# Kernel tuning notes

Hardware: AMD Instinct MI355X
Metric: run time of the kernel (lower is better)

The kernel has to match this reference:

```python
import jax, jax.numpy as jnp
import numpy as np

N_GROUP = 8
TOPK_GROUP = 4
TOP_K = 8
ROUTED_SCALING = 2.5
NUM_EXPERTS = 256
HIDDEN = 7168
TOKENS = 8192


def setup_inputs() -> dict:
    key = jax.random.key(0)
    k1, k2, k3 = jax.random.split(key, 3)
    hidden_states = jax.random.normal(k1, (TOKENS, HIDDEN), dtype=jnp.float32)
    weight = jax.random.normal(k2, (NUM_EXPERTS, HIDDEN), dtype=jnp.float32) * 0.02
    e_score_correction_bias = jax.random.normal(k3, (NUM_EXPERTS,), dtype=jnp.float32) * 0.1
    return {"hidden_states": hidden_states, "weight": weight,
            "e_score_correction_bias": e_score_correction_bias}


def reference(hidden_states, weight, e_score_correction_bias):
    # logits = x @ W^T  (fp32 gate GEMM)
    logits = jnp.einsum('th,eh->te', hidden_states.astype(jnp.float32), weight)
    scores = jax.nn.sigmoid(logits)                       # [T, E]
    swb = scores + e_score_correction_bias                # [T, E]
    T, E = swb.shape
    gsize = E // N_GROUP
    # per-group score = sum of top-2 biased scores within each group
    grouped = swb.reshape(T, N_GROUP, gsize)
    top2, _ = jax.lax.top_k(grouped, 2)                   # [T, G, 2]
    group_scores = top2.sum(axis=-1)                      # [T, G]
    # keep topk_group groups
    _, gidx = jax.lax.top_k(group_scores, TOPK_GROUP)     # [T, topk_group]
    rows = jnp.arange(T)[:, None]
    group_mask = jnp.zeros((T, N_GROUP), jnp.float32).at[rows, gidx].set(1.0)
    score_mask = jnp.repeat(group_mask, gsize, axis=-1)   # [T, E]
    swb_masked = swb * score_mask
    # top_k experts among kept groups
    _, tidx = jax.lax.top_k(swb_masked, TOP_K)            # [T, top_k]
    new_mask = jnp.zeros((T, E), jnp.float32).at[rows, tidx].set(1.0)
    sel = scores * new_mask
    score_sum = sel.sum(axis=-1, keepdims=True) + 1e-20
    return sel / score_sum * ROUTED_SCALING
```

## Files before the change

### kernel.cpp

```cpp
#include <hip/hip_runtime.h>
#include <math.h>

#define TOKENS   8192
#define HIDDEN   7168
#define NEXPERT  256
#define NGROUP   8
#define TOPKG    4
#define TOPK     8
#define SCALE    2.5f

#define BM 128
#define BN 128
#define BK 32
#define KSPLIT 4
#define KPB (HIDDEN / KSPLIT)
#define NT  (KPB / BK)

#define RSTR 72

typedef _Float16 half8 __attribute__((ext_vector_type(8)));
typedef _Float16 half4 __attribute__((ext_vector_type(4)));
typedef float    floatx4 __attribute__((ext_vector_type(4)));

__device__ __forceinline__ void cvt_store(_Float16* __restrict__ H,
                                          int row, int k0, float4 v) {
    half4 h, l;
    h[0] = (_Float16)v.x; h[1] = (_Float16)v.y;
    h[2] = (_Float16)v.z; h[3] = (_Float16)v.w;
    l[0] = (_Float16)(v.x - (float)h[0]);
    l[1] = (_Float16)(v.y - (float)h[1]);
    l[2] = (_Float16)(v.z - (float)h[2]);
    l[3] = (_Float16)(v.w - (float)h[3]);
    const int base = row * RSTR + ((k0 >> 3) << 4) + (k0 & 7);
    *(half4*)&H[base]     = h;
    *(half4*)&H[base + 8] = l;
}

__global__ __launch_bounds__(256) void zero_kernel(float* __restrict__ O) {
    const int i = blockIdx.x * 256 + threadIdx.x;
    *(float4*)&O[(size_t)i * 4] = float4{0.f, 0.f, 0.f, 0.f};
}

__global__ __launch_bounds__(256, 2) void gate_gemm_kernel(
    const float* __restrict__ X, const float* __restrict__ W,
    float* __restrict__ OUT)
{
    __shared__ _Float16 Ab[2][BM * RSTR];
    __shared__ _Float16 Bb[2][BN * RSTR];

    const int tid = threadIdx.x;
    const int nb  = blockIdx.x * BN;
    const int mb  = blockIdx.y * BM;
    const int kb  = blockIdx.z * KPB;

    const int srow = tid >> 3;
    const int sk0  = (tid & 7) * 4;
    const float* Aptr = X + (size_t)(mb + srow) * HIDDEN + kb + sk0;
    const float* Bptr = W + (size_t)(nb + srow) * HIDDEN + kb + sk0;

    float4 av[4], bv[4];
#pragma unroll
    for (int q = 0; q < 4; q++) {
        av[q] = *(const float4*)(Aptr + (size_t)(q * 32) * HIDDEN);
        bv[q] = *(const float4*)(Bptr + (size_t)(q * 32) * HIDDEN);
    }
#pragma unroll
    for (int q = 0; q < 4; q++) {
        cvt_store(Ab[0], q * 32 + srow, sk0, av[q]);
        cvt_store(Bb[0], q * 32 + srow, sk0, bv[q]);
    }

    const int lane = tid & 63, wave = tid >> 6;
    const int wm = (wave >> 1) * 64, wn = (wave & 1) * 64;
    const int fr = lane & 15, quad = lane >> 4;

    floatx4 acc[4][4];
#pragma unroll
    for (int i = 0; i < 4; i++)
#pragma unroll
        for (int j = 0; j < 4; j++) acc[i][j] = floatx4{0.f, 0.f, 0.f, 0.f};

    for (int t = 0; t < NT; t++) {
        if (t + 1 < NT) {
            const int o = (t + 1) * BK;
#pragma unroll
            for (int q = 0; q < 4; q++) {
                av[q] = *(const float4*)(Aptr + o + (size_t)(q * 32) * HIDDEN);
                bv[q] = *(const float4*)(Bptr + o + (size_t)(q * 32) * HIDDEN);
            }
        }

        __syncthreads();

        const _Float16* __restrict__ Ac = Ab[t & 1];
        const _Float16* __restrict__ Bc = Bb[t & 1];

        half8 ah[4], al[4];
#pragma unroll
        for (int i = 0; i < 4; i++) {
            const int a = (wm + i * 16 + fr) * RSTR + quad * 16;
            ah[i] = *(const half8*)&Ac[a];
            al[i] = *(const half8*)&Ac[a + 8];
        }
#pragma unroll
        for (int j = 0; j < 4; j++) {
            const int b = (wn + j * 16 + fr) * RSTR + quad * 16;
            const half8 bh = *(const half8*)&Bc[b];
            const half8 bl = *(const half8*)&Bc[b + 8];
#pragma unroll
            for (int i = 0; i < 4; i++) {
                acc[i][j] = __builtin_amdgcn_mfma_f32_16x16x32_f16(
                    al[i], bh, acc[i][j], 0, 0, 0);
                acc[i][j] = __builtin_amdgcn_mfma_f32_16x16x32_f16(
                    ah[i], bl, acc[i][j], 0, 0, 0);
                acc[i][j] = __builtin_amdgcn_mfma_f32_16x16x32_f16(
                    ah[i], bh, acc[i][j], 0, 0, 0);
            }
        }

        if (t + 1 < NT) {
            _Float16* An = Ab[(t + 1) & 1];
            _Float16* Bn = Bb[(t + 1) & 1];
#pragma unroll
            for (int q = 0; q < 4; q++) {
                cvt_store(An, q * 32 + srow, sk0, av[q]);
                cvt_store(Bn, q * 32 + srow, sk0, bv[q]);
            }
        }
    }

#pragma unroll
    for (int i = 0; i < 4; i++)
#pragma unroll
        for (int j = 0; j < 4; j++) {
            const int col = nb + wn + j * 16 + fr;
#pragma unroll
            for (int r = 0; r < 4; r++) {
                const int row = mb + wm + i * 16 + quad * 4 + r;
                atomicAdd(&OUT[(size_t)row * NEXPERT + col], acc[i][j][r]);
            }
        }
}

__global__ __launch_bounds__(256) void route_kernel(
    float* __restrict__ S, const float* __restrict__ bias)
{
    const int lane = threadIdx.x & 63;
    const int wave = threadIdx.x >> 6;
    const int t    = blockIdx.x * 4 + wave;

    const float4 lg4 = *(const float4*)&S[(size_t)t * NEXPERT + lane * 4];
    const float4 b4  = *(const float4*)&bias[lane * 4];
    float sc[4];
    sc[0] = 1.0f / (1.0f + expf(-lg4.x));
    sc[1] = 1.0f / (1.0f + expf(-lg4.y));
    sc[2] = 1.0f / (1.0f + expf(-lg4.z));
    sc[3] = 1.0f / (1.0f + expf(-lg4.w));
    float swb[4] = { sc[0] + b4.x, sc[1] + b4.y, sc[2] + b4.z, sc[3] + b4.w };

    float m1 = -INFINITY, m2 = -INFINITY;
#pragma unroll
    for (int j = 0; j < 4; j++) {
        const float v = swb[j];
        if (v > m1)      { m2 = m1; m1 = v; }
        else if (v > m2) { m2 = v; }
    }
#pragma unroll
    for (int s = 1; s < 8; s <<= 1) {
        const float o1 = __shfl_xor(m1, s, 64);
        const float o2 = __shfl_xor(m2, s, 64);
        const float hi = fmaxf(m1, o1);
        const float lo = fminf(m1, o1);
        m2 = fmaxf(lo, fmaxf(m2, o2));
        m1 = hi;
    }
    const float gs = m1 + m2;

    float gsc[NGROUP];
#pragma unroll
    for (int g = 0; g < NGROUP; g++) gsc[g] = __shfl(gs, g * 8, 64);
    const int myg = lane >> 3;
    int rank = 0;
#pragma unroll
    for (int g = 0; g < NGROUP; g++)
        rank += (gsc[g] > gs) || (gsc[g] == gs && g < myg);
    const bool kept = (rank < TOPKG);

    float v[4];
#pragma unroll
    for (int j = 0; j < 4; j++) v[j] = kept ? swb[j] : 0.0f;

    float sum = 0.0f;
    int selmask = 0;
    for (int r = 0; r < TOPK; r++) {
        float bv = -INFINITY;
        int   bi = 0x7fffffff;
#pragma unroll
        for (int j = 0; j < 4; j++) {
            const bool avail = ((selmask >> j) & 1) == 0;
            if (avail && v[j] > bv) { bv = v[j]; bi = lane * 4 + j; }
        }
#pragma unroll
        for (int s = 1; s < 64; s <<= 1) {
            const float ov = __shfl_xor(bv, s, 64);
            const int   oi = __shfl_xor(bi, s, 64);
            if (ov > bv || (ov == bv && oi < bi)) { bv = ov; bi = oi; }
        }
        const int wl = bi >> 2, wj = bi & 3;
        const float mysc = (wj == 0) ? sc[0] : (wj == 1) ? sc[1]
                         : (wj == 2) ? sc[2] : sc[3];
        sum += __shfl(mysc, wl, 64);
        if (lane == wl) selmask |= (1 << wj);
    }

    const float rcp = SCALE / (sum + 1e-20f);
    float4 o;
    o.x = (selmask & 1) ? sc[0] * rcp : 0.0f;
    o.y = (selmask & 2) ? sc[1] * rcp : 0.0f;
    o.z = (selmask & 4) ? sc[2] * rcp : 0.0f;
    o.w = (selmask & 8) ? sc[3] * rcp : 0.0f;
    *(float4*)&S[(size_t)t * NEXPERT + lane * 4] = o;
}

extern "C" void kernel_launch(void* const* d_in, const int* in_sizes, int n_in,
                              void* d_out, int out_size, void* d_ws, size_t ws_size,
                              hipStream_t stream) {
    const float* X    = (const float*)d_in[0];
    const float* W    = (const float*)d_in[1];
    const float* bias = (const float*)d_in[2];
    float* out = (float*)d_out;
    (void)d_ws; (void)ws_size;

    zero_kernel<<<(TOKENS * NEXPERT / 4) / 256, 256, 0, stream>>>(out);
    dim3 ggrid(NEXPERT / BN, TOKENS / BM, KSPLIT);
    gate_gemm_kernel<<<ggrid, 256, 0, stream>>>(X, W, out);
    route_kernel<<<TOKENS / 4, 256, 0, stream>>>(out, bias);
}
```

Before: 374.5 us.

## Deepen global prefetch to two tiles ahead in gate GEMM loop

Restructures the split-K gate GEMM main loop to keep two register sets of prefetched global tiles, loading tile t+2 while computing tile t, with the loop manually unrolled by two over the LDS double buffer. This is meant to hide more global memory latency behind the MFMA work. In exchange it uses 32 more VGPRs for the extra float4 buffers, which may reduce occupancy under launch_bounds(256,2) or cause spills. NT = 56 is even, so the unroll-by-two covers every tile.

```diff
diff --git a/kernel.cpp b/kernel.cpp
--- a/kernel.cpp
+++ b/kernel.cpp
@@ -58,18 +58,6 @@
     const float* Aptr = X + (size_t)(mb + srow) * HIDDEN + kb + sk0;
     const float* Bptr = W + (size_t)(nb + srow) * HIDDEN + kb + sk0;
 
-    float4 av[4], bv[4];
-#pragma unroll
-    for (int q = 0; q < 4; q++) {
-        av[q] = *(const float4*)(Aptr + (size_t)(q * 32) * HIDDEN);
-        bv[q] = *(const float4*)(Bptr + (size_t)(q * 32) * HIDDEN);
-    }
-#pragma unroll
-    for (int q = 0; q < 4; q++) {
-        cvt_store(Ab[0], q * 32 + srow, sk0, av[q]);
-        cvt_store(Bb[0], q * 32 + srow, sk0, bv[q]);
-    }
-
     const int lane = tid & 63, wave = tid >> 6;
     const int wm = (wave >> 1) * 64, wn = (wave & 1) * 64;
     const int fr = lane & 15, quad = lane >> 4;
@@ -80,21 +68,26 @@
 #pragma unroll
         for (int j = 0; j < 4; j++) acc[i][j] = floatx4{0.f, 0.f, 0.f, 0.f};
 
-    for (int t = 0; t < NT; t++) {
-        if (t + 1 < NT) {
-            const int o = (t + 1) * BK;
-#pragma unroll
-            for (int q = 0; q < 4; q++) {
-                av[q] = *(const float4*)(Aptr + o + (size_t)(q * 32) * HIDDEN);
-                bv[q] = *(const float4*)(Bptr + o + (size_t)(q * 32) * HIDDEN);
-            }
-        }
-
-        __syncthreads();
-
-        const _Float16* __restrict__ Ac = Ab[t & 1];
-        const _Float16* __restrict__ Bc = Bb[t & 1];
-
+    float4 av0[4], bv0[4], av1[4], bv1[4];
+
+    auto load_tile = [&](float4* av, float4* bv, int t) {
+        const int o = t * BK;
+#pragma unroll
+        for (int q = 0; q < 4; q++) {
+            av[q] = *(const float4*)(Aptr + o + (size_t)(q * 32) * HIDDEN);
+            bv[q] = *(const float4*)(Bptr + o + (size_t)(q * 32) * HIDDEN);
+        }
+    };
+    auto stage = [&](_Float16* A, _Float16* B, const float4* av,
+                     const float4* bv) {
+#pragma unroll
+        for (int q = 0; q < 4; q++) {
+            cvt_store(A, q * 32 + srow, sk0, av[q]);
+            cvt_store(B, q * 32 + srow, sk0, bv[q]);
+        }
+    };
+    auto compute = [&](const _Float16* __restrict__ Ac,
+                       const _Float16* __restrict__ Bc) {
         half8 ah[4], al[4];
 #pragma unroll
         for (int i = 0; i < 4; i++) {
@@ -117,16 +110,23 @@
                     ah[i], bh, acc[i][j], 0, 0, 0);
             }
         }
-
-        if (t + 1 < NT) {
-            _Float16* An = Ab[(t + 1) & 1];
-            _Float16* Bn = Bb[(t + 1) & 1];
-#pragma unroll
-            for (int q = 0; q < 4; q++) {
-                cvt_store(An, q * 32 + srow, sk0, av[q]);
-                cvt_store(Bn, q * 32 + srow, sk0, bv[q]);
-            }
-        }
+    };
+
+    load_tile(av0, bv0, 0);
+    load_tile(av1, bv1, 1);
+    stage(Ab[0], Bb[0], av0, bv0);
+
+#pragma unroll 1
+    for (int t = 0; t < NT; t += 2) {
+        __syncthreads();
+        if (t + 2 < NT) load_tile(av0, bv0, t + 2);
+        compute(Ab[0], Bb[0]);
+        stage(Ab[1], Bb[1], av1, bv1);
+
+        __syncthreads();
+        if (t + 3 < NT) load_tile(av1, bv1, t + 3);
+        compute(Ab[1], Bb[1]);
+        if (t + 2 < NT) stage(Ab[0], Bb[0], av0, bv0);
     }
 
 #pragma unroll
```

After: 385.7 us. +3.0%, slower.
